# Performance work log

Measured on AMD Instinct MI355X. Metric: run time of the kernel, lower is better.

## Reference

```python
import jax, jax.numpy as jnp
import numpy as np

NUM_HEADS = 16


def setup_inputs() -> dict:
    key = jax.random.key(0)
    ks = jax.random.split(key, 6)
    B, SQ, SC, E = 2, 2048, 2048, 1024
    x = jax.random.normal(ks[0], (B, SQ, E), dtype=jnp.float32)
    cache = jax.random.normal(ks[1], (B, SC, E), dtype=jnp.float32)
    in_proj_w = jax.random.normal(ks[2], (3 * E, E), dtype=jnp.float32) * 0.02
    in_proj_b = jnp.zeros((3 * E,), dtype=jnp.float32)
    out_proj_w = jax.random.normal(ks[3], (E, E), dtype=jnp.float32) * 0.02
    out_proj_b = jnp.zeros((E,), dtype=jnp.float32)
    return {"x": x, "cache": cache, "in_proj_w": in_proj_w, "in_proj_b": in_proj_b,
            "out_proj_w": out_proj_w, "out_proj_b": out_proj_b}


def reference(x, cache, in_proj_w, in_proj_b, out_proj_w, out_proj_b):
    # k = v = cat([cache, x], dim=1); then torch MultiheadAttention(x, k, v)
    B, SQ, E = x.shape
    H = NUM_HEADS
    D = E // H
    kv = jnp.concatenate([cache, x], axis=1)  # [B, SKV, E]
    SKV = kv.shape[1]
    # packed in_proj: rows [0:E]=Wq, [E:2E]=Wk, [2E:3E]=Wv (torch layout: y = x @ W.T + b)
    q = x @ in_proj_w[:E].T + in_proj_b[:E]
    k = kv @ in_proj_w[E:2 * E].T + in_proj_b[E:2 * E]
    v = kv @ in_proj_w[2 * E:].T + in_proj_b[2 * E:]
    q = q.reshape(B, SQ, H, D)
    k = k.reshape(B, SKV, H, D)
    v = v.reshape(B, SKV, H, D)
    scale = 1.0 / jnp.sqrt(jnp.asarray(D, dtype=q.dtype))
    scores = jnp.einsum("bqhd,bkhd->bhqk", q, k) * scale  # [B,H,SQ,SKV]
    attn = jax.nn.softmax(scores, axis=-1)
    ctx = jnp.einsum("bhqk,bkhd->bqhd", attn, v).reshape(B, SQ, E)
    out = ctx @ out_proj_w.T + out_proj_b
    return out
```

## Files before the change

### kernel.cpp

```cpp
#include <hip/hip_runtime.h>
#include <stdint.h>

typedef __attribute__((ext_vector_type(4))) float f32x4;
typedef __attribute__((ext_vector_type(16))) float f32x16;
typedef __attribute__((ext_vector_type(8))) __bf16 bf16x8v;

#define E_DIM 1024
#define H_NUM 16
#define D_DIM 64
#define SQ_LEN 2048
#define SKV_LEN 4096

static __device__ __forceinline__ unsigned short f2bf(float f) {
  union { float f; unsigned u; } v; v.f = f;
  unsigned u = v.u;
  u += 0x7fffu + ((u >> 16) & 1u);
  return (unsigned short)(u >> 16);
}

static __device__ __forceinline__ float bfu2f(unsigned u16) {
  union { unsigned u; float f; } v; v.u = u16 << 16; return v.f;
}

static __device__ __forceinline__ float exp2_fast(float x) {
#if __has_builtin(__builtin_amdgcn_exp2f)
  return __builtin_amdgcn_exp2f(x);
#else
  return exp2f(x);
#endif
}

static __device__ __forceinline__ unsigned cvt_pk_bf16(float lo, float hi) {
  unsigned r;
  asm("v_cvt_pk_bf16_f32 %0, %1, %2" : "=v"(r) : "v"(lo), "v"(hi));
  return r;
}

static __device__ __forceinline__ void plswap(unsigned &a, unsigned &b) {
#if __has_builtin(__builtin_amdgcn_permlane32_swap)
  auto r = __builtin_amdgcn_permlane32_swap(a, b, false, false);
  a = r[0]; b = r[1];
#else
  asm volatile("v_permlane32_swap_b32 %0, %1" : "+v"(a), "+v"(b));
#endif
}

static __device__ __forceinline__ void gload_lds16(const unsigned short* g, unsigned short* l) {
  __builtin_amdgcn_global_load_lds(
      (const __attribute__((address_space(1))) unsigned int*)g,
      (__attribute__((address_space(3))) unsigned int*)l,
      16, 0, 0);
}

__global__ __launch_bounds__(256)
void convert_all(const float* __restrict__ x, const float* __restrict__ cache,
                 const float* __restrict__ in_w, const float* __restrict__ out_w,
                 unsigned short* __restrict__ dst) {
  int i = blockIdx.x * 256 + threadIdx.x;
  const float* src;
  int rel;
  if (i < 2097152) {
    if (i < 1048576) { src = x; rel = i; }
    else { src = cache; rel = i - 1048576; }
  } else {
    if (i < 2883584) { src = in_w; rel = i - 2097152; }
    else { src = out_w; rel = i - 2883584; }
  }
  const float4 f = *reinterpret_cast<const float4*>(src + rel * 4);
  ushort4 o;
  o.x = f2bf(f.x); o.y = f2bf(f.y); o.z = f2bf(f.z); o.w = f2bf(f.w);
  *reinterpret_cast<ushort4*>(dst + (size_t)i * 4) = o;
}

__global__ __launch_bounds__(512, 4)
void qkv_gemm(const unsigned short* __restrict__ xb,
              const unsigned short* __restrict__ cb,
              const unsigned short* __restrict__ wqkv,
              const float* __restrict__ in_b,
              unsigned short* __restrict__ Qo,
              unsigned short* __restrict__ Ko,
              unsigned short* __restrict__ Vo) {
  const int bid = blockIdx.x;
  int job, mt, nt;
  if (bid < 256) {
    int c = bid & 7, l = bid >> 3;
    job = 0; mt = (l >> 3) * 8 + c; nt = l & 7;
  } else {
    int i = bid - 256;
    int c = i & 7, l = i >> 3;
    job = 1 + (l & 1);
    nt = (l >> 1) & 7;
    mt = (l >> 4) * 8 + c;
  }

  __shared__ unsigned short As[128 * 64];
  __shared__ unsigned short Bs[128 * 64];

  const int t = threadIdx.x;
  const int lane = t & 63, wave = t >> 6;
  const int g = lane >> 4, lr = lane & 15;
  const int wr = (wave >> 2) * 64, wc = (wave & 3) * 32;
  const int m0 = mt * 128, n0 = nt * 128;

  const unsigned short* arow[2];
  const unsigned short* brow[2];
  int col[2];
  const unsigned short* wbase = wqkv + job * (E_DIM * E_DIM);
#pragma unroll
  for (int i = 0; i < 2; ++i) {
    int f = i * 512 + t;
    int row = f >> 3, grp = f & 7;
    int gm = m0 + row;
    const unsigned short* src;
    if (job == 0) {
      src = xb + gm * E_DIM;
    } else {
      int b = gm >> 12, s = gm & 4095;
      src = (s < 2048) ? (cb + (b * 2048 + s) * E_DIM)
                       : (xb + (b * 2048 + (s - 2048)) * E_DIM);
    }
    arow[i] = src;
    brow[i] = wbase + (n0 + row) * E_DIM;
    col[i] = (grp ^ (row & 7)) * 8;
  }

  f32x4 acc[4][2];
#pragma unroll
  for (int i = 0; i < 4; ++i)
#pragma unroll
    for (int j = 0; j < 2; ++j) acc[i][j] = f32x4{0.f, 0.f, 0.f, 0.f};

  for (int k0 = 0; k0 < E_DIM; k0 += 64) {
#pragma unroll
    for (int i = 0; i < 2; ++i) {
      unsigned ldsoff = (unsigned)((i * 512 + t) * 16);
      gload_lds16(arow[i] + k0 + col[i], (unsigned short*)((char*)As + ldsoff));
      gload_lds16(brow[i] + k0 + col[i], (unsigned short*)((char*)Bs + ldsoff));
    }
    __syncthreads();
#pragma unroll
    for (int ks = 0; ks < 2; ++ks) {
      bf16x8v a[4], b[2];
#pragma unroll
      for (int mf = 0; mf < 4; ++mf) {
        int row = wr + mf * 16 + lr;
        unsigned byte = (unsigned)(row * 128 + ks * 64 + g * 16) ^ (unsigned)((row & 7) << 4);
        a[mf] = *reinterpret_cast<const bf16x8v*>((const char*)As + byte);
      }
#pragma unroll
      for (int nf = 0; nf < 2; ++nf) {
        int row = wc + nf * 16 + lr;
        unsigned byte = (unsigned)(row * 128 + ks * 64 + g * 16) ^ (unsigned)((row & 7) << 4);
        b[nf] = *reinterpret_cast<const bf16x8v*>((const char*)Bs + byte);
      }
#pragma unroll
      for (int mf = 0; mf < 4; ++mf)
#pragma unroll
        for (int nf = 0; nf < 2; ++nf)
          acc[mf][nf] = __builtin_amdgcn_mfma_f32_16x16x32_bf16(a[mf], b[nf], acc[mf][nf], 0, 0, 0);
    }
    __syncthreads();
  }

  const float* bptr = in_b + job * E_DIM;
  const float qscale = 0.125f * 1.44269504088896f;
#pragma unroll
  for (int mf = 0; mf < 4; ++mf) {
#pragma unroll
    for (int nf = 0; nf < 2; ++nf) {
      int n = n0 + wc + nf * 16 + lr;
      float bv = bptr[n];
      int h = n >> 6, d = n & 63;
#pragma unroll
      for (int r = 0; r < 4; ++r) {
        int m = m0 + wr + mf * 16 + g * 4 + r;
        float val = acc[mf][nf][r] + bv;
        if (job == 0) {
          int b = m >> 11, s = m & 2047;
          Qo[((b * H_NUM + h) * SQ_LEN + s) * D_DIM + d] = f2bf(val * qscale);
        } else if (job == 1) {
          int b = m >> 12, s = m & 4095;
          Ko[((b * H_NUM + h) * SKV_LEN + s) * D_DIM + d] = f2bf(val);
        } else {
          int b = m >> 12, s = m & 4095;
          Vo[((b * H_NUM + h) * D_DIM + d) * SKV_LEN + s] = f2bf(val);
        }
      }
    }
  }
}

__global__ __launch_bounds__(512, 4)
void attn_kernel(const unsigned short* __restrict__ Qb,
                 const unsigned short* __restrict__ Kb,
                 const unsigned short* __restrict__ Vb,
                 unsigned short* __restrict__ po,
                 float* __restrict__ pl) {
  const int swz = (blockIdx.x & 7) * 64 + (blockIdx.x >> 3);
  const int qt = swz & 7;
  const int bh = (swz >> 3) & 31;
  const int ck = swz >> 8;

  __shared__ unsigned short Ks[2][4096];
  __shared__ unsigned short Vs[2][4096];

  const int t = threadIdx.x;
  const int lane = t & 63, wave = t >> 6;
  const int hi = lane >> 5, l31 = lane & 31;

  const unsigned short* Qh = Qb + (size_t)bh * SQ_LEN * D_DIM;
  const unsigned short* Kh = Kb + (size_t)bh * SKV_LEN * D_DIM;
  const unsigned short* Vh = Vb + (size_t)bh * D_DIM * SKV_LEN;

  const int q0 = qt * 256 + wave * 32;
  const int kvb = ck * 2048;

  bf16x8v qfr[4];
#pragma unroll
  for (int ks = 0; ks < 4; ++ks)
    qfr[ks] = *reinterpret_cast<const bf16x8v*>(Qh + (q0 + l31) * D_DIM + ks * 16 + hi * 8);

  const int shi = t & 1, sl31 = (t >> 1) & 31, skvh = (t >> 6) & 1, sks = t >> 7;
  const int kOff = (skvh * 32 + sl31) * D_DIM + sks * 16 + shi * 8;
  const int vOff = (skvh * 32 + sl31) * SKV_LEN + sks * 16 + shi * 8;
  const unsigned ldsoff = (unsigned)(t * 16);

  f32x16 o0, o1;
#pragma unroll
  for (int i = 0; i < 16; ++i) { o0[i] = 0.f; o1[i] = 0.f; }
  float lsum = 0.f;

  gload_lds16(Kh + (size_t)kvb * D_DIM + kOff, (unsigned short*)((char*)Ks[0] + ldsoff));
  gload_lds16(Vh + kvb + vOff, (unsigned short*)((char*)Vs[0] + ldsoff));
  __syncthreads();

  int cur = 0;
  for (int tkv = 0; tkv < 32; ++tkv) {
    if (tkv + 1 < 32) {
      int kv0 = kvb + (tkv + 1) * 64;
      gload_lds16(Kh + (size_t)kv0 * D_DIM + kOff, (unsigned short*)((char*)Ks[cur ^ 1] + ldsoff));
      gload_lds16(Vh + kv0 + vOff, (unsigned short*)((char*)Vs[cur ^ 1] + ldsoff));
    }

    f32x16 st0, st1;
#pragma unroll
    for (int i = 0; i < 16; ++i) { st0[i] = 0.f; st1[i] = 0.f; }
#pragma unroll
    for (int ks = 0; ks < 4; ++ks) {
      unsigned b0 = (unsigned)(ks * 2048 + l31 * 32 + hi * 16);
      bf16x8v kf0 = *reinterpret_cast<const bf16x8v*>((const char*)Ks[cur] + b0);
      bf16x8v kf1 = *reinterpret_cast<const bf16x8v*>((const char*)Ks[cur] + b0 + 1024);
      __builtin_amdgcn_s_setprio(1);
      st0 = __builtin_amdgcn_mfma_f32_32x32x16_bf16(kf0, qfr[ks], st0, 0, 0, 0);
      st1 = __builtin_amdgcn_mfma_f32_32x32x16_bf16(kf1, qfr[ks], st1, 0, 0, 0);
      __builtin_amdgcn_s_setprio(0);
    }

    unsigned c[16];
#pragma unroll
    for (int k = 0; k < 8; ++k) {
      float e0 = exp2_fast(st0[2 * k]), e1 = exp2_fast(st0[2 * k + 1]);
      lsum += e0 + e1;
      c[k] = cvt_pk_bf16(e0, e1);
    }
#pragma unroll
    for (int k = 0; k < 8; ++k) {
      float e0 = exp2_fast(st1[2 * k]), e1 = exp2_fast(st1[2 * k + 1]);
      lsum += e0 + e1;
      c[8 + k] = cvt_pk_bf16(e0, e1);
    }
    plswap(c[0], c[2]);  plswap(c[1], c[3]);
    plswap(c[4], c[6]);  plswap(c[5], c[7]);
    plswap(c[8], c[10]); plswap(c[9], c[11]);
    plswap(c[12], c[14]); plswap(c[13], c[15]);
    bf16x8v pa[4];
#pragma unroll
    for (int ks = 0; ks < 4; ++ks) {
      union { unsigned u[4]; bf16x8v v; } w;
      w.u[0] = c[4 * ks + 0]; w.u[1] = c[4 * ks + 1];
      w.u[2] = c[4 * ks + 2]; w.u[3] = c[4 * ks + 3];
      pa[ks] = w.v;
    }

#pragma unroll
    for (int ks = 0; ks < 4; ++ks) {
      unsigned b0 = (unsigned)(ks * 2048 + l31 * 32 + hi * 16);
      bf16x8v vf0 = *reinterpret_cast<const bf16x8v*>((const char*)Vs[cur] + b0);
      bf16x8v vf1 = *reinterpret_cast<const bf16x8v*>((const char*)Vs[cur] + b0 + 1024);
      __builtin_amdgcn_s_setprio(1);
      o0 = __builtin_amdgcn_mfma_f32_32x32x16_bf16(pa[ks], vf0, o0, 0, 0, 0);
      o1 = __builtin_amdgcn_mfma_f32_32x32x16_bf16(pa[ks], vf1, o1, 0, 0, 0);
      __builtin_amdgcn_s_setprio(0);
    }
    __syncthreads();
    cur ^= 1;
  }

  lsum += __shfl_xor(lsum, 32, 64);

  const size_t rowb = ((size_t)(ck * 32 + bh) * SQ_LEN + q0);
#pragma unroll
  for (int reg = 0; reg < 16; ++reg) {
    int crow = (reg & 3) + 8 * (reg >> 2) + 4 * hi;
    float linv = 1.0f / __shfl(lsum, crow, 64);
    po[(rowb + crow) * D_DIM + l31]      = f2bf(o0[reg] * linv);
    po[(rowb + crow) * D_DIM + 32 + l31] = f2bf(o1[reg] * linv);
  }
  if (lane < 32) pl[rowb + lane] = lsum;
}

__global__ __launch_bounds__(256)
void combine_kernel(const unsigned short* __restrict__ po,
                    const float* __restrict__ pl,
                    unsigned short* __restrict__ cx) {
  int idx = blockIdx.x * 256 + threadIdx.x;
  int d8 = idx & 7;
  int q  = (idx >> 3) & 2047;
  int bh = idx >> 14;
  size_t base = (size_t)bh * SQ_LEN + q;
  const size_t CS = (size_t)32 * SQ_LEN;
  float l0 = pl[base], l1 = pl[CS + base];
  float inv = 1.0f / (l0 + l1);
  float w0 = l0 * inv, w1 = l1 * inv;
  const uint4 v0 = *reinterpret_cast<const uint4*>(po + base * D_DIM + d8 * 8);
  const uint4 v1 = *reinterpret_cast<const uint4*>(po + CS * D_DIM + base * D_DIM + d8 * 8);
  const unsigned* u0 = (const unsigned*)&v0;
  const unsigned* u1 = (const unsigned*)&v1;
  uint4 r;
  unsigned* ru = (unsigned*)&r;
#pragma unroll
  for (int i = 0; i < 4; ++i) {
    float lo = bfu2f(u0[i] & 0xffffu) * w0 + bfu2f(u1[i] & 0xffffu) * w1;
    float hh = bfu2f(u0[i] >> 16) * w0 + bfu2f(u1[i] >> 16) * w1;
    ru[i] = ((unsigned)f2bf(hh) << 16) | (unsigned)f2bf(lo);
  }
  size_t co = ((size_t)(bh >> 4) * SQ_LEN + q) * E_DIM + (bh & 15) * D_DIM + d8 * 8;
  *reinterpret_cast<uint4*>(cx + co) = r;
}

__global__ __launch_bounds__(512, 4)
void out_gemm(const unsigned short* __restrict__ cx,
              const unsigned short* __restrict__ wo,
              const float* __restrict__ ob,
              float* __restrict__ out) {
  const int bid = blockIdx.x;
  const int cX = bid & 7, lX = bid >> 3;
  const int mt = (lX >> 3) * 8 + cX;
  const int nt = lX & 7;

  __shared__ unsigned short As[128 * 64];
  __shared__ unsigned short Bs[128 * 64];

  const int t = threadIdx.x;
  const int lane = t & 63, wave = t >> 6;
  const int g = lane >> 4, lr = lane & 15;
  const int wr = (wave >> 2) * 64, wc = (wave & 3) * 32;
  const int m0 = mt * 128, n0 = nt * 128;

  const unsigned short* arow[2];
  const unsigned short* brow[2];
  int col[2];
#pragma unroll
  for (int i = 0; i < 2; ++i) {
    int f = i * 512 + t;
    int row = f >> 3, grp = f & 7;
    arow[i] = cx + (m0 + row) * E_DIM;
    brow[i] = wo + (n0 + row) * E_DIM;
    col[i] = (grp ^ (row & 7)) * 8;
  }

  f32x4 acc[4][2];
#pragma unroll
  for (int i = 0; i < 4; ++i)
#pragma unroll
    for (int j = 0; j < 2; ++j) acc[i][j] = f32x4{0.f, 0.f, 0.f, 0.f};

  for (int k0 = 0; k0 < E_DIM; k0 += 64) {
#pragma unroll
    for (int i = 0; i < 2; ++i) {
      unsigned ldsoff = (unsigned)((i * 512 + t) * 16);
      gload_lds16(arow[i] + k0 + col[i], (unsigned short*)((char*)As + ldsoff));
      gload_lds16(brow[i] + k0 + col[i], (unsigned short*)((char*)Bs + ldsoff));
    }
    __syncthreads();
#pragma unroll
    for (int ks = 0; ks < 2; ++ks) {
      bf16x8v a[4], b[2];
#pragma unroll
      for (int mf = 0; mf < 4; ++mf) {
        int row = wr + mf * 16 + lr;
        unsigned byte = (unsigned)(row * 128 + ks * 64 + g * 16) ^ (unsigned)((row & 7) << 4);
        a[mf] = *reinterpret_cast<const bf16x8v*>((const char*)As + byte);
      }
#pragma unroll
      for (int nf = 0; nf < 2; ++nf) {
        int row = wc + nf * 16 + lr;
        unsigned byte = (unsigned)(row * 128 + ks * 64 + g * 16) ^ (unsigned)((row & 7) << 4);
        b[nf] = *reinterpret_cast<const bf16x8v*>((const char*)Bs + byte);
      }
#pragma unroll
      for (int mf = 0; mf < 4; ++mf)
#pragma unroll
        for (int nf = 0; nf < 2; ++nf)
          acc[mf][nf] = __builtin_amdgcn_mfma_f32_16x16x32_bf16(a[mf], b[nf], acc[mf][nf], 0, 0, 0);
    }
    __syncthreads();
  }

#pragma unroll
  for (int mf = 0; mf < 4; ++mf) {
#pragma unroll
    for (int nf = 0; nf < 2; ++nf) {
      int n = n0 + wc + nf * 16 + lr;
      float bv = ob[n];
#pragma unroll
      for (int r = 0; r < 4; ++r) {
        int m = m0 + wr + mf * 16 + g * 4 + r;
        out[(size_t)m * E_DIM + n] = acc[mf][nf][r] + bv;
      }
    }
  }
}

extern "C" void kernel_launch(void* const* d_in, const int* in_sizes, int n_in,
                              void* d_out, int out_size, void* d_ws, size_t ws_size,
                              hipStream_t stream) {
  (void)in_sizes; (void)n_in; (void)out_size; (void)ws_size;
  const float* x     = (const float*)d_in[0];
  const float* cache = (const float*)d_in[1];
  const float* in_w  = (const float*)d_in[2];
  const float* in_b  = (const float*)d_in[3];
  const float* out_w = (const float*)d_in[4];
  const float* out_b = (const float*)d_in[5];
  float* out = (float*)d_out;

  char* ws = (char*)d_ws;
  unsigned short* xb   = (unsigned short*)(ws);
  unsigned short* cb   = (unsigned short*)(ws + (8u  << 20));
  unsigned short* wqkv = (unsigned short*)(ws + (16u << 20));
  unsigned short* wo   = (unsigned short*)(ws + (22u << 20));
  unsigned short* Qb   = (unsigned short*)(ws + (24u << 20));
  unsigned short* Kb   = (unsigned short*)(ws + (32u << 20));
  unsigned short* Vb   = (unsigned short*)(ws + (48u << 20));
  unsigned short* cx   = (unsigned short*)(ws + (64u << 20));
  unsigned short* po = (unsigned short*)(ws);
  float* pl = (float*)(ws + (16u << 20));

  convert_all<<<12288, 256, 0, stream>>>(x, cache, in_w, out_w, (unsigned short*)ws);

  qkv_gemm<<<1280, 512, 0, stream>>>(xb, cb, wqkv, in_b, Qb, Kb, Vb);
  attn_kernel<<<dim3(512), 512, 0, stream>>>(Qb, Kb, Vb, po, pl);
  combine_kernel<<<2048, 256, 0, stream>>>(po, pl, cx);
  out_gemm<<<256, 512, 0, stream>>>(cx, wo, out_b, out);
}
```

Baseline: 192.3 us.

## Double-buffer GEMM LDS tiles with vmcnt barriers and vectorize V stores

The QKV and output GEMMs now use double-buffered LDS tiles. The next K-slice is prefetched via global_load_lds while the current slice feeds MFMAs, and the full __syncthreads is replaced by s_waitcnt vmcnt(N) plus s_barrier so only the older loads must land. The attention loop gets the same partial-wait barriers, and MFMA sections are given raised priority with s_setprio. V-projection output stores are packed into 8-byte ushort4 writes along the sequence dimension instead of four scalar stores. This doubles LDS use per block, which may reduce occupancy, and it relies on the hand-written vmcnt counts being exact. The last iteration issues a redundant reload so the wait count stays uniform.

```diff
diff --git a/kernel.cpp b/kernel.cpp
--- a/kernel.cpp
+++ b/kernel.cpp
@@ -51,6 +51,10 @@
       (__attribute__((address_space(3))) unsigned int*)l,
       16, 0, 0);
 }
+
+#define BAR_WAIT4() asm volatile("s_waitcnt vmcnt(4)\ns_barrier" ::: "memory")
+#define BAR_WAIT2() asm volatile("s_waitcnt vmcnt(2)\ns_barrier" ::: "memory")
+#define BAR_END()   asm volatile("s_waitcnt lgkmcnt(0)\ns_barrier" ::: "memory")
 
 __global__ __launch_bounds__(256)
 void convert_all(const float* __restrict__ x, const float* __restrict__ cache,
@@ -93,8 +97,8 @@
     mt = (l >> 4) * 8 + c;
   }
 
-  __shared__ unsigned short As[128 * 64];
-  __shared__ unsigned short Bs[128 * 64];
+  __shared__ unsigned short As[2][128 * 64];
+  __shared__ unsigned short Bs[2][128 * 64];
 
   const int t = threadIdx.x;
   const int lane = t & 63, wave = t >> 6;
@@ -130,14 +134,26 @@
 #pragma unroll
     for (int j = 0; j < 2; ++j) acc[i][j] = f32x4{0.f, 0.f, 0.f, 0.f};
 
-  for (int k0 = 0; k0 < E_DIM; k0 += 64) {
+#pragma unroll
+  for (int i = 0; i < 2; ++i) {
+    unsigned off = (unsigned)((i * 512 + t) * 16);
+    gload_lds16(arow[i] + col[i], (unsigned short*)((char*)As[0] + off));
+    gload_lds16(brow[i] + col[i], (unsigned short*)((char*)Bs[0] + off));
+  }
+
+  int cur = 0;
+  for (int kt = 0; kt < 16; ++kt) {
+    int nk = (kt + 1 < 16) ? (kt + 1) * 64 : kt * 64;
 #pragma unroll
     for (int i = 0; i < 2; ++i) {
-      unsigned ldsoff = (unsigned)((i * 512 + t) * 16);
-      gload_lds16(arow[i] + k0 + col[i], (unsigned short*)((char*)As + ldsoff));
-      gload_lds16(brow[i] + k0 + col[i], (unsigned short*)((char*)Bs + ldsoff));
-    }
-    __syncthreads();
+      unsigned off = (unsigned)((i * 512 + t) * 16);
+      gload_lds16(arow[i] + nk + col[i], (unsigned short*)((char*)As[cur ^ 1] + off));
+      gload_lds16(brow[i] + nk + col[i], (unsigned short*)((char*)Bs[cur ^ 1] + off));
+    }
+    BAR_WAIT4();
+
+    const char* Ab = (const char*)As[cur];
+    const char* Bb = (const char*)Bs[cur];
 #pragma unroll
     for (int ks = 0; ks < 2; ++ks) {
       bf16x8v a[4], b[2];
@@ -145,21 +161,24 @@
       for (int mf = 0; mf < 4; ++mf) {
         int row = wr + mf * 16 + lr;
         unsigned byte = (unsigned)(row * 128 + ks * 64 + g * 16) ^ (unsigned)((row & 7) << 4);
-        a[mf] = *reinterpret_cast<const bf16x8v*>((const char*)As + byte);
+        a[mf] = *reinterpret_cast<const bf16x8v*>(Ab + byte);
       }
 #pragma unroll
       for (int nf = 0; nf < 2; ++nf) {
         int row = wc + nf * 16 + lr;
         unsigned byte = (unsigned)(row * 128 + ks * 64 + g * 16) ^ (unsigned)((row & 7) << 4);
-        b[nf] = *reinterpret_cast<const bf16x8v*>((const char*)Bs + byte);
-      }
+        b[nf] = *reinterpret_cast<const bf16x8v*>(Bb + byte);
+      }
+      __builtin_amdgcn_s_setprio(1);
 #pragma unroll
       for (int mf = 0; mf < 4; ++mf)
 #pragma unroll
         for (int nf = 0; nf < 2; ++nf)
           acc[mf][nf] = __builtin_amdgcn_mfma_f32_16x16x32_bf16(a[mf], b[nf], acc[mf][nf], 0, 0, 0);
-    }
-    __syncthreads();
+      __builtin_amdgcn_s_setprio(0);
+    }
+    BAR_END();
+    cur ^= 1;
   }
 
   const float* bptr = in_b + job * E_DIM;
@@ -171,19 +190,27 @@
       int n = n0 + wc + nf * 16 + lr;
       float bv = bptr[n];
       int h = n >> 6, d = n & 63;
-#pragma unroll
-      for (int r = 0; r < 4; ++r) {
-        int m = m0 + wr + mf * 16 + g * 4 + r;
-        float val = acc[mf][nf][r] + bv;
-        if (job == 0) {
-          int b = m >> 11, s = m & 2047;
-          Qo[((b * H_NUM + h) * SQ_LEN + s) * D_DIM + d] = f2bf(val * qscale);
-        } else if (job == 1) {
-          int b = m >> 12, s = m & 4095;
-          Ko[((b * H_NUM + h) * SKV_LEN + s) * D_DIM + d] = f2bf(val);
-        } else {
-          int b = m >> 12, s = m & 4095;
-          Vo[((b * H_NUM + h) * D_DIM + d) * SKV_LEN + s] = f2bf(val);
+      if (job == 2) {
+        int m = m0 + wr + mf * 16 + g * 4;
+        int b = m >> 12, s = m & 4095;
+        ushort4 pk;
+        pk.x = f2bf(acc[mf][nf][0] + bv);
+        pk.y = f2bf(acc[mf][nf][1] + bv);
+        pk.z = f2bf(acc[mf][nf][2] + bv);
+        pk.w = f2bf(acc[mf][nf][3] + bv);
+        *reinterpret_cast<ushort4*>(&Vo[(size_t)((b * H_NUM + h) * D_DIM + d) * SKV_LEN + s]) = pk;
+      } else {
+#pragma unroll
+        for (int r = 0; r < 4; ++r) {
+          int m = m0 + wr + mf * 16 + g * 4 + r;
+          float val = acc[mf][nf][r] + bv;
+          if (job == 0) {
+            int b = m >> 11, s = m & 2047;
+            Qo[((b * H_NUM + h) * SQ_LEN + s) * D_DIM + d] = f2bf(val * qscale);
+          } else {
+            int b = m >> 12, s = m & 4095;
+            Ko[((b * H_NUM + h) * SKV_LEN + s) * D_DIM + d] = f2bf(val);
+          }
         }
       }
     }
@@ -232,15 +259,13 @@
 
   gload_lds16(Kh + (size_t)kvb * D_DIM + kOff, (unsigned short*)((char*)Ks[0] + ldsoff));
   gload_lds16(Vh + kvb + vOff, (unsigned short*)((char*)Vs[0] + ldsoff));
-  __syncthreads();
 
   int cur = 0;
   for (int tkv = 0; tkv < 32; ++tkv) {
-    if (tkv + 1 < 32) {
-      int kv0 = kvb + (tkv + 1) * 64;
-      gload_lds16(Kh + (size_t)kv0 * D_DIM + kOff, (unsigned short*)((char*)Ks[cur ^ 1] + ldsoff));
-      gload_lds16(Vh + kv0 + vOff, (unsigned short*)((char*)Vs[cur ^ 1] + ldsoff));
-    }
+    int nk = (tkv + 1 < 32) ? kvb + (tkv + 1) * 64 : kvb + tkv * 64;
+    gload_lds16(Kh + (size_t)nk * D_DIM + kOff, (unsigned short*)((char*)Ks[cur ^ 1] + ldsoff));
+    gload_lds16(Vh + nk + vOff, (unsigned short*)((char*)Vs[cur ^ 1] + ldsoff));
+    BAR_WAIT2();
 
     f32x16 st0, st1;
 #pragma unroll
@@ -292,7 +317,7 @@
       o1 = __builtin_amdgcn_mfma_f32_32x32x16_bf16(pa[ks], vf1, o1, 0, 0, 0);
       __builtin_amdgcn_s_setprio(0);
     }
-    __syncthreads();
+    BAR_END();
     cur ^= 1;
   }
 
@@ -348,8 +373,8 @@
   const int mt = (lX >> 3) * 8 + cX;
   const int nt = lX & 7;
 
-  __shared__ unsigned short As[128 * 64];
-  __shared__ unsigned short Bs[128 * 64];
+  __shared__ unsigned short As[2][128 * 64];
+  __shared__ unsigned short Bs[2][128 * 64];
 
   const int t = threadIdx.x;
   const int lane = t & 63, wave = t >> 6;
@@ -375,14 +400,26 @@
 #pragma unroll
     for (int j = 0; j < 2; ++j) acc[i][j] = f32x4{0.f, 0.f, 0.f, 0.f};
 
-  for (int k0 = 0; k0 < E_DIM; k0 += 64) {
+#pragma unroll
+  for (int i = 0; i < 2; ++i) {
+    unsigned off = (unsigned)((i * 512 + t) * 16);
+    gload_lds16(arow[i] + col[i], (unsigned short*)((char*)As[0] + off));
+    gload_lds16(brow[i] + col[i], (unsigned short*)((char*)Bs[0] + off));
+  }
+
+  int cur = 0;
+  for (int kt = 0; kt < 16; ++kt) {
+    int nk = (kt + 1 < 16) ? (kt + 1) * 64 : kt * 64;
 #pragma unroll
     for (int i = 0; i < 2; ++i) {
-      unsigned ldsoff = (unsigned)((i * 512 + t) * 16);
-      gload_lds16(arow[i] + k0 + col[i], (unsigned short*)((char*)As + ldsoff));
-      gload_lds16(brow[i] + k0 + col[i], (unsigned short*)((char*)Bs + ldsoff));
-    }
-    __syncthreads();
+      unsigned off = (unsigned)((i * 512 + t) * 16);
+      gload_lds16(arow[i] + nk + col[i], (unsigned short*)((char*)As[cur ^ 1] + off));
+      gload_lds16(brow[i] + nk + col[i], (unsigned short*)((char*)Bs[cur ^ 1] + off));
+    }
+    BAR_WAIT4();
+
+    const char* Ab = (const char*)As[cur];
+    const char* Bb = (const char*)Bs[cur];
 #pragma unroll
     for (int ks = 0; ks < 2; ++ks) {
       bf16x8v a[4], b[2];
@@ -390,21 +427,24 @@
       for (int mf = 0; mf < 4; ++mf) {
         int row = wr + mf * 16 + lr;
         unsigned byte = (unsigned)(row * 128 + ks * 64 + g * 16) ^ (unsigned)((row & 7) << 4);
-        a[mf] = *reinterpret_cast<const bf16x8v*>((const char*)As + byte);
+        a[mf] = *reinterpret_cast<const bf16x8v*>(Ab + byte);
       }
 #pragma unroll
       for (int nf = 0; nf < 2; ++nf) {
         int row = wc + nf * 16 + lr;
         unsigned byte = (unsigned)(row * 128 + ks * 64 + g * 16) ^ (unsigned)((row & 7) << 4);
-        b[nf] = *reinterpret_cast<const bf16x8v*>((const char*)Bs + byte);
-      }
+        b[nf] = *reinterpret_cast<const bf16x8v*>(Bb + byte);
+      }
+      __builtin_amdgcn_s_setprio(1);
 #pragma unroll
       for (int mf = 0; mf < 4; ++mf)
 #pragma unroll
         for (int nf = 0; nf < 2; ++nf)
           acc[mf][nf] = __builtin_amdgcn_mfma_f32_16x16x32_bf16(a[mf], b[nf], acc[mf][nf], 0, 0, 0);
-    }
-    __syncthreads();
+      __builtin_amdgcn_s_setprio(0);
+    }
+    BAR_END();
+    cur ^= 1;
   }
 
 #pragma unroll
```

Result: faster. 166.3 us (-13.5%).
